# Kernel optimization log

Measured on AMD Instinct MI355X. Metric: run time of the kernel, lower is better.

Reference implementation:

```python
import jax, jax.numpy as jnp
import numpy as np

B, S, HID = 4, 2048, 576
NH, NKV, HD = 9, 3, 64
MAXPOS, THETA = 8192, 100000.0


def rotate_half(x):
    x1, x2 = x[..., : x.shape[-1] // 2], x[..., x.shape[-1] // 2 :]
    return jnp.concatenate((-x2, x1), axis=-1)


def setup_inputs() -> dict:
    key = jax.random.key(0)
    ks = jax.random.split(key, 6)
    x = jax.random.normal(ks[0], (B, S, HID), dtype=jnp.float32)
    # RoPE tables (HuggingFace layout: freqs duplicated across halves)
    inv_freq = 1.0 / (THETA ** (np.arange(0, HD, 2, dtype=np.float32) / HD))
    freqs = np.outer(np.arange(MAXPOS, dtype=np.float32), inv_freq)
    emb = np.concatenate([freqs, freqs], axis=-1)
    cos = jnp.asarray(np.cos(emb))
    sin = jnp.asarray(np.sin(emb))
    position_ids = jnp.broadcast_to(jnp.arange(S, dtype=jnp.int64), (B, S))
    # additive causal mask [B,1,S,S]
    causal = jnp.where(
        jnp.tril(jnp.ones((S, S), dtype=bool)), 0.0, -1e9
    ).astype(jnp.float32)
    attention_mask = jnp.broadcast_to(causal, (B, 1, S, S))
    scale = 0.02
    wq = jax.random.normal(ks[1], (NH * HD, HID), dtype=jnp.float32) * scale
    wk = jax.random.normal(ks[2], (NKV * HD, HID), dtype=jnp.float32) * scale
    wv = jax.random.normal(ks[3], (NKV * HD, HID), dtype=jnp.float32) * scale
    wo = jax.random.normal(ks[4], (HID, NH * HD), dtype=jnp.float32) * scale
    return {
        "x": x, "cos": cos, "sin": sin, "position_ids": position_ids,
        "attention_mask": attention_mask,
        "wq": wq, "wk": wk, "wv": wv, "wo": wo,
    }


def reference(x, cos, sin, position_ids, attention_mask, wq, wk, wv, wo):
    b, s, _ = x.shape
    # projections (nn.Linear: y = x @ W.T), split into heads -> [B,H,S,D]
    q = (x @ wq.T).reshape(b, s, NH, HD).transpose(0, 2, 1, 3)
    k = (x @ wk.T).reshape(b, s, NKV, HD).transpose(0, 2, 1, 3)
    v = (x @ wv.T).reshape(b, s, NKV, HD).transpose(0, 2, 1, 3)
    # RoPE: cos/sin gathered per position -> [B,1,S,D], broadcast over heads
    c = cos[position_ids][:, None, :, :]
    si = sin[position_ids][:, None, :, :]
    q = q * c + rotate_half(q) * si
    k = k * c + rotate_half(k) * si
    # GQA expansion: repeat_interleave kv heads to match q heads
    k = jnp.repeat(k, NH // NKV, axis=1)
    v = jnp.repeat(v, NH // NKV, axis=1)
    scale = 1.0 / jnp.sqrt(jnp.asarray(HD, dtype=x.dtype))
    scores = jnp.einsum("bhqd,bhkd->bhqk", q, k) * scale + attention_mask
    attn = jax.nn.softmax(scores.astype(jnp.float32), axis=-1).astype(q.dtype)
    out = jnp.einsum("bhqk,bhkd->bhqd", attn, v)
    out = out.transpose(0, 2, 1, 3).reshape(b, s, NH * HD)
    return out @ wo.T
```

## Files before the change

### kernel.cpp

```cpp
#include <hip/hip_runtime.h>
#include <hip/hip_bf16.h>

#define B_    4
#define S_    2048
#define HID_  576
#define NH_   9
#define NKV_  3
#define HD_   64
#define GQ_   3

typedef __attribute__((ext_vector_type(8))) short bf16x8;
typedef __attribute__((ext_vector_type(4))) float f32x4;

__device__ __forceinline__ short f2bf(float f) {
    union { float f; unsigned int u; } v; v.f = f;
    unsigned int r = (v.u + 0x7fffu + ((v.u >> 16) & 1u)) >> 16;
    return (short)r;
}

__device__ __forceinline__ void async16(const void* g, void* l) {
    __builtin_amdgcn_global_load_lds(
        (const __attribute__((address_space(1))) unsigned int*)g,
        (__attribute__((address_space(3))) unsigned int*)l, 16, 0, 0);
}

#define NX_   (8192 * 576)
#define NWQ_  (576 * 576)
#define NWK_  (192 * 576)
#define NWV_  (192 * 576)
#define NWO_  (576 * 576)
#define NTOT_ (NX_ + NWQ_ + NWK_ + NWV_ + NWO_)

__global__ __launch_bounds__(256) void convert_kernel(
    const float* __restrict__ x,  const float* __restrict__ wq,
    const float* __restrict__ wk, const float* __restrict__ wv,
    const float* __restrict__ wo,
    short* __restrict__ xb, short* __restrict__ wqkvb, short* __restrict__ wob)
{
    int i4 = (blockIdx.x * 256 + threadIdx.x) * 4;
    const float* src; short* dst;
    if (i4 < NX_)                          { src = x  + i4;                          dst = xb    + i4; }
    else if (i4 < NX_ + NWQ_)              { src = wq + (i4 - NX_);                  dst = wqkvb + (i4 - NX_); }
    else if (i4 < NX_ + NWQ_ + NWK_)       { src = wk + (i4 - NX_ - NWQ_);           dst = wqkvb + (i4 - NX_); }
    else if (i4 < NX_ + NWQ_ + NWK_ + NWV_){ src = wv + (i4 - NX_ - NWQ_ - NWK_);    dst = wqkvb + (i4 - NX_); }
    else                                   { src = wo + (i4 - NX_ - NWQ_ - NWK_ - NWV_);
                                             dst = wob + (i4 - NX_ - NWQ_ - NWK_ - NWV_); }
    float4 v = *(const float4*)src;
    short4 o = make_short4(f2bf(v.x), f2bf(v.y), f2bf(v.z), f2bf(v.w));
    *(short4*)dst = o;
}

__global__ __launch_bounds__(256) void qkv_kernel(
    const short* __restrict__ xb,
    const short* __restrict__ wqkvb,
    const float* __restrict__ cosb,
    const float* __restrict__ sinb,
    short* __restrict__ Q,
    short* __restrict__ K,
    short* __restrict__ Vt)
{
    __shared__ __align__(16) short As[128 * 64];
    __shared__ __align__(16) short Bs[64 * 64];

    const int m0     = blockIdx.x * 128;
    const int nb_blk = blockIdx.y;
    const int tid  = threadIdx.x;
    const int w    = tid >> 6, lane = tid & 63;
    const int quad = lane >> 4, c = lane & 15;
    const int lr   = lane >> 3, lg = lane & 7;
    const int sw   = lg ^ lr;
    const int xg   = quad ^ (c & 7);

    f32x4 acc[2][4];
    #pragma unroll
    for (int mf = 0; mf < 2; ++mf)
        #pragma unroll
        for (int nb = 0; nb < 4; ++nb) acc[mf][nb] = (f32x4){0.f, 0.f, 0.f, 0.f};

    for (int kk = 0; kk < 9; ++kk) {
        const int k0 = kk * 64;
        __syncthreads();
        #pragma unroll
        for (int r = 0; r < 4; ++r) {
            int ch = w * 4 + r;
            int R  = ch * 8 + lr;
            async16(xb + (size_t)(m0 + R) * HID_ + k0 + sw * 8,
                    (char*)As + ch * 1024);
        }
        #pragma unroll
        for (int r = 0; r < 2; ++r) {
            int ch = w * 2 + r;
            int R  = ch * 8 + lr;
            async16(wqkvb + (size_t)(nb_blk * 64 + R) * HID_ + k0 + sw * 8,
                    (char*)Bs + ch * 1024);
        }
        __syncthreads();

        bf16x8 a[2][2], bfr[4][2];
        #pragma unroll
        for (int mf = 0; mf < 2; ++mf) {
            int row = w * 32 + mf * 16 + c;
            a[mf][0] = *(const bf16x8*)(As + row * 64 + xg * 8);
            a[mf][1] = *(const bf16x8*)(As + row * 64 + (xg ^ 4) * 8);
        }
        #pragma unroll
        for (int nb = 0; nb < 4; ++nb) {
            int row = nb * 16 + c;
            bfr[nb][0] = *(const bf16x8*)(Bs + row * 64 + xg * 8);
            bfr[nb][1] = *(const bf16x8*)(Bs + row * 64 + (xg ^ 4) * 8);
        }
        #pragma unroll
        for (int mf = 0; mf < 2; ++mf)
            #pragma unroll
            for (int nb = 0; nb < 4; ++nb) {
                acc[mf][nb] = __builtin_amdgcn_mfma_f32_16x16x32_bf16(a[mf][0], bfr[nb][0], acc[mf][nb], 0, 0, 0);
                acc[mf][nb] = __builtin_amdgcn_mfma_f32_16x16x32_bf16(a[mf][1], bfr[nb][1], acc[mf][nb], 0, 0, 0);
            }
    }

    int type, head;
    if (nb_blk < NH_)            { type = 0; head = nb_blk; }
    else if (nb_blk < NH_ + NKV_){ type = 1; head = nb_blk - NH_; }
    else                         { type = 2; head = nb_blk - NH_ - NKV_; }
    const int b  = m0 >> 11;
    const int s0 = m0 & (S_ - 1);

    if (type < 2) {
        #pragma unroll
        for (int mf = 0; mf < 2; ++mf)
            #pragma unroll
            for (int reg = 0; reg < 4; ++reg) {
                int s = s0 + w * 32 + mf * 16 + quad * 4 + reg;
                const float* cr = cosb + (size_t)s * HD_;
                const float* sr = sinb + (size_t)s * HD_;
                float a0 = acc[mf][0][reg], a1 = acc[mf][1][reg];
                float a2 = acc[mf][2][reg], a3 = acc[mf][3][reg];
                float o0 = a0 * cr[c]      - a2 * sr[c];
                float o1 = a1 * cr[c + 16] - a3 * sr[c + 16];
                float o2 = a2 * cr[c + 32] + a0 * sr[c + 32];
                float o3 = a3 * cr[c + 48] + a1 * sr[c + 48];
                short* dst = (type == 0)
                    ? Q + (((size_t)b * NH_  + head) * S_ + s) * HD_
                    : K + (((size_t)b * NKV_ + head) * S_ + s) * HD_;
                dst[c]      = f2bf(o0);
                dst[c + 16] = f2bf(o1);
                dst[c + 32] = f2bf(o2);
                dst[c + 48] = f2bf(o3);
            }
    } else {
        short* base = Vt + (((size_t)b * NKV_ + head) * HD_) * S_;
        #pragma unroll
        for (int mf = 0; mf < 2; ++mf) {
            int s4 = s0 + w * 32 + mf * 16 + quad * 4;
            #pragma unroll
            for (int nb = 0; nb < 4; ++nb) {
                int d = nb * 16 + c;
                short4 pk = make_short4(f2bf(acc[mf][nb][0]), f2bf(acc[mf][nb][1]),
                                        f2bf(acc[mf][nb][2]), f2bf(acc[mf][nb][3]));
                *(short4*)(base + (size_t)d * S_ + s4) = pk;
            }
        }
    }
}

__global__ __launch_bounds__(256) void attn_kernel(
    const short* __restrict__ Q,
    const short* __restrict__ K,
    const short* __restrict__ Vt,
    short* __restrict__ AOb)
{
    __shared__ __align__(16) short Qs[64 * 64];
    __shared__ __align__(16) short Ks[2][64 * 64];
    __shared__ __align__(16) short Vs[2][64 * 64];
    __shared__ __align__(16) short Ps[64][72];

    const int hb = blockIdx.x;
    const int h  = hb >> 2, b = hb & 3;
    const int qt = 31 - blockIdx.y;
    const int kh = h / GQ_;
    const int tid  = threadIdx.x;
    const int w    = tid >> 6, lane = tid & 63;
    const int quad = lane >> 4, c = lane & 15;
    const int lr   = lane >> 3, lg = lane & 7;
    const int sw   = lg ^ lr;
    const int xg   = quad ^ (c & 7);

    const short* Qg = Q  + (((size_t)b * NH_  + h ) * S_ + qt * 64) * HD_;
    const short* Kg = K  + (((size_t)b * NKV_ + kh) * S_) * HD_;
    const short* Vg = Vt + (((size_t)b * NKV_ + kh) * HD_) * S_;

    #pragma unroll
    for (int r = 0; r < 2; ++r) {
        int ch = w * 2 + r;
        int R  = ch * 8 + lr;
        async16(Qg + (size_t)R * HD_ + sw * 8, (char*)Qs + ch * 1024);
    }
    #pragma unroll
    for (int r = 0; r < 4; ++r) {
        int it = w * 4 + r;
        if (it < 8) {
            int R = it * 8 + lr;
            async16(Kg + (size_t)R * HD_ + sw * 8, (char*)Ks[0] + it * 1024);
        } else {
            int R = (it - 8) * 8 + lr;
            async16(Vg + (size_t)R * S_ + sw * 8, (char*)Vs[0] + (it - 8) * 1024);
        }
    }

    f32x4 acc_o[4];
    #pragma unroll
    for (int nb = 0; nb < 4; ++nb) acc_o[nb] = (f32x4){0.f, 0.f, 0.f, 0.f};
    float mrow[4], lrow[4];
    #pragma unroll
    for (int r = 0; r < 4; ++r) { mrow[r] = -1e30f; lrow[r] = 0.f; }

    const float scale = 0.125f;
    int buf = 0;

    for (int kt = 0; kt <= qt; ++kt) {
        __syncthreads();
        if (kt < qt) {
            int nxt = buf ^ 1;
            #pragma unroll
            for (int r = 0; r < 4; ++r) {
                int it = w * 4 + r;
                if (it < 8) {
                    int R = it * 8 + lr;
                    async16(Kg + (size_t)((kt + 1) * 64 + R) * HD_ + sw * 8,
                            (char*)Ks[nxt] + it * 1024);
                } else {
                    int R = (it - 8) * 8 + lr;
                    async16(Vg + (size_t)R * S_ + (kt + 1) * 64 + sw * 8,
                            (char*)Vs[nxt] + (it - 8) * 1024);
                }
            }
        }
        const short* ks = Ks[buf];
        const short* vs = Vs[buf];

        bf16x8 aq0 = *(const bf16x8*)(Qs + (w * 16 + c) * 64 + xg * 8);
        bf16x8 aq1 = *(const bf16x8*)(Qs + (w * 16 + c) * 64 + (xg ^ 4) * 8);
        f32x4 sc[4];
        #pragma unroll
        for (int nb = 0; nb < 4; ++nb) {
            bf16x8 bk0 = *(const bf16x8*)(ks + (nb * 16 + c) * 64 + xg * 8);
            bf16x8 bk1 = *(const bf16x8*)(ks + (nb * 16 + c) * 64 + (xg ^ 4) * 8);
            f32x4 z = (f32x4){0.f, 0.f, 0.f, 0.f};
            z = __builtin_amdgcn_mfma_f32_16x16x32_bf16(aq0, bk0, z, 0, 0, 0);
            z = __builtin_amdgcn_mfma_f32_16x16x32_bf16(aq1, bk1, z, 0, 0, 0);
            sc[nb] = z;
        }

        const bool diag = (kt == qt);
        #pragma unroll
        for (int r = 0; r < 4; ++r) {
            const int qrow = w * 16 + quad * 4 + r;
            float v[4];
            float rmax = -1e30f;
            #pragma unroll
            for (int nb = 0; nb < 4; ++nb) {
                float sv = sc[nb][r] * scale;
                if (diag && (nb * 16 + c > qrow)) sv = -1e30f;
                v[nb] = sv;
                rmax = fmaxf(rmax, sv);
            }
            rmax = fmaxf(rmax, __shfl_xor(rmax, 1));
            rmax = fmaxf(rmax, __shfl_xor(rmax, 2));
            rmax = fmaxf(rmax, __shfl_xor(rmax, 4));
            rmax = fmaxf(rmax, __shfl_xor(rmax, 8));
            float mnew  = fmaxf(mrow[r], rmax);
            float alpha = __expf(mrow[r] - mnew);
            mrow[r] = mnew;
            float rsum = 0.f;
            #pragma unroll
            for (int nb = 0; nb < 4; ++nb) {
                float p = __expf(v[nb] - mnew);
                rsum += p;
                Ps[w * 16 + quad * 4 + r][nb * 16 + c] = f2bf(p);
            }
            rsum += __shfl_xor(rsum, 1);
            rsum += __shfl_xor(rsum, 2);
            rsum += __shfl_xor(rsum, 4);
            rsum += __shfl_xor(rsum, 8);
            lrow[r] = lrow[r] * alpha + rsum;
            #pragma unroll
            for (int nb = 0; nb < 4; ++nb) acc_o[nb][r] *= alpha;
        }

        #pragma unroll
        for (int kc = 0; kc < 2; ++kc) {
            bf16x8 ap = *(const bf16x8*)&Ps[w * 16 + c][quad * 8 + kc * 32];
            int pg = kc ? (xg ^ 4) : xg;
            #pragma unroll
            for (int nb = 0; nb < 4; ++nb) {
                bf16x8 bv = *(const bf16x8*)(vs + (nb * 16 + c) * 64 + pg * 8);
                acc_o[nb] = __builtin_amdgcn_mfma_f32_16x16x32_bf16(ap, bv, acc_o[nb], 0, 0, 0);
            }
        }
        buf ^= 1;
    }

    #pragma unroll
    for (int r = 0; r < 4; ++r) {
        int s = qt * 64 + w * 16 + quad * 4 + r;
        float inv = 1.f / lrow[r];
        short* dst = AOb + (((size_t)b * S_ + s) * NH_ + h) * HD_;
        #pragma unroll
        for (int nb = 0; nb < 4; ++nb)
            dst[nb * 16 + c] = f2bf(acc_o[nb][r] * inv);
    }
}

__global__ __launch_bounds__(256) void oproj_kernel(
    const short* __restrict__ AOb,
    const short* __restrict__ wob,
    float* __restrict__ out)
{
    __shared__ __align__(16) short As[128 * 64];
    __shared__ __align__(16) short Bs[64 * 64];

    const int m0 = blockIdx.x * 128;
    const int n0 = blockIdx.y * 64;
    const int tid  = threadIdx.x;
    const int w    = tid >> 6, lane = tid & 63;
    const int quad = lane >> 4, c = lane & 15;
    const int lr   = lane >> 3, lg = lane & 7;
    const int sw   = lg ^ lr;
    const int xg   = quad ^ (c & 7);

    f32x4 acc[2][4];
    #pragma unroll
    for (int mf = 0; mf < 2; ++mf)
        #pragma unroll
        for (int nb = 0; nb < 4; ++nb) acc[mf][nb] = (f32x4){0.f, 0.f, 0.f, 0.f};

    for (int kk = 0; kk < 9; ++kk) {
        const int k0 = kk * 64;
        __syncthreads();
        #pragma unroll
        for (int r = 0; r < 4; ++r) {
            int ch = w * 4 + r;
            int R  = ch * 8 + lr;
            async16(AOb + (size_t)(m0 + R) * HID_ + k0 + sw * 8,
                    (char*)As + ch * 1024);
        }
        #pragma unroll
        for (int r = 0; r < 2; ++r) {
            int ch = w * 2 + r;
            int R  = ch * 8 + lr;
            async16(wob + (size_t)(n0 + R) * HID_ + k0 + sw * 8,
                    (char*)Bs + ch * 1024);
        }
        __syncthreads();

        bf16x8 a[2][2], bfr[4][2];
        #pragma unroll
        for (int mf = 0; mf < 2; ++mf) {
            int row = w * 32 + mf * 16 + c;
            a[mf][0] = *(const bf16x8*)(As + row * 64 + xg * 8);
            a[mf][1] = *(const bf16x8*)(As + row * 64 + (xg ^ 4) * 8);
        }
        #pragma unroll
        for (int nb = 0; nb < 4; ++nb) {
            int row = nb * 16 + c;
            bfr[nb][0] = *(const bf16x8*)(Bs + row * 64 + xg * 8);
            bfr[nb][1] = *(const bf16x8*)(Bs + row * 64 + (xg ^ 4) * 8);
        }
        #pragma unroll
        for (int mf = 0; mf < 2; ++mf)
            #pragma unroll
            for (int nb = 0; nb < 4; ++nb) {
                acc[mf][nb] = __builtin_amdgcn_mfma_f32_16x16x32_bf16(a[mf][0], bfr[nb][0], acc[mf][nb], 0, 0, 0);
                acc[mf][nb] = __builtin_amdgcn_mfma_f32_16x16x32_bf16(a[mf][1], bfr[nb][1], acc[mf][nb], 0, 0, 0);
            }
    }

    #pragma unroll
    for (int mf = 0; mf < 2; ++mf)
        #pragma unroll
        for (int reg = 0; reg < 4; ++reg) {
            int m = m0 + w * 32 + mf * 16 + quad * 4 + reg;
            float* dst = out + (size_t)m * HID_ + n0;
            #pragma unroll
            for (int nb = 0; nb < 4; ++nb)
                dst[nb * 16 + c] = acc[mf][nb][reg];
        }
}

extern "C" void kernel_launch(void* const* d_in, const int* in_sizes, int n_in,
                              void* d_out, int out_size, void* d_ws, size_t ws_size,
                              hipStream_t stream) {
    const float* x    = (const float*)d_in[0];
    const float* cosb = (const float*)d_in[1];
    const float* sinb = (const float*)d_in[2];
    const float* wq   = (const float*)d_in[5];
    const float* wk   = (const float*)d_in[6];
    const float* wv   = (const float*)d_in[7];
    const float* wo   = (const float*)d_in[8];

    short* xb    = (short*)d_ws;
    short* wqkvb = xb    + (size_t)NX_;
    short* wob   = wqkvb + (size_t)(NWQ_ + NWK_ + NWV_);
    short* Qb    = wob   + (size_t)NWO_;
    short* Kb    = Qb    + (size_t)B_ * NH_  * S_ * HD_;
    short* Vtb   = Kb    + (size_t)B_ * NKV_ * S_ * HD_;
    short* AOb   = Vtb   + (size_t)B_ * NKV_ * S_ * HD_;

    convert_kernel<<<dim3(NTOT_ / 4 / 256), dim3(256), 0, stream>>>(
        x, wq, wk, wv, wo, xb, wqkvb, wob);
    qkv_kernel<<<dim3(64, 15), dim3(256), 0, stream>>>(
        xb, wqkvb, cosb, sinb, Qb, Kb, Vtb);
    attn_kernel<<<dim3(36, 32), dim3(256), 0, stream>>>(Qb, Kb, Vtb, AOb);
    oproj_kernel<<<dim3(64, 9), dim3(256), 0, stream>>>(AOb, wob, (float*)d_out);
}
```

Before: 215.0 us.

## Enlarge attention query tile to 128 rows and double-buffer GEMM loads

The attention kernel now handles 128 query rows per block, with each warp owning 32 rows. Every K/V tile loaded into shared memory is therefore reused across twice as many queries. Q is kept in registers so its shared buffer can be reused for the softmax probabilities, and the causal mask now covers the two diagonal KV tiles. Separately, the QKV and output-projection GEMMs double-buffer their A/B tiles, prefetching the next K slice during the current MFMAs. The costs are half as many attention blocks, which risks worse load balance on the causal grid, and higher register and LDS use per block.

```diff
diff --git a/kernel.cpp b/kernel.cpp
--- a/kernel.cpp
+++ b/kernel.cpp
@@ -59,8 +59,8 @@
     short* __restrict__ K,
     short* __restrict__ Vt)
 {
-    __shared__ __align__(16) short As[128 * 64];
-    __shared__ __align__(16) short Bs[64 * 64];
+    __shared__ __align__(16) short As[2][128 * 64];
+    __shared__ __align__(16) short Bs[2][64 * 64];
 
     const int m0     = blockIdx.x * 128;
     const int nb_blk = blockIdx.y;
@@ -77,37 +77,48 @@
         #pragma unroll
         for (int nb = 0; nb < 4; ++nb) acc[mf][nb] = (f32x4){0.f, 0.f, 0.f, 0.f};
 
+    #pragma unroll
+    for (int r = 0; r < 4; ++r) {
+        int ch = w * 4 + r, R = ch * 8 + lr;
+        async16(xb + (size_t)(m0 + R) * HID_ + sw * 8, (char*)As[0] + ch * 1024);
+    }
+    #pragma unroll
+    for (int r = 0; r < 2; ++r) {
+        int ch = w * 2 + r, R = ch * 8 + lr;
+        async16(wqkvb + (size_t)(nb_blk * 64 + R) * HID_ + sw * 8, (char*)Bs[0] + ch * 1024);
+    }
+
+    int buf = 0;
     for (int kk = 0; kk < 9; ++kk) {
-        const int k0 = kk * 64;
         __syncthreads();
-        #pragma unroll
-        for (int r = 0; r < 4; ++r) {
-            int ch = w * 4 + r;
-            int R  = ch * 8 + lr;
-            async16(xb + (size_t)(m0 + R) * HID_ + k0 + sw * 8,
-                    (char*)As + ch * 1024);
-        }
-        #pragma unroll
-        for (int r = 0; r < 2; ++r) {
-            int ch = w * 2 + r;
-            int R  = ch * 8 + lr;
-            async16(wqkvb + (size_t)(nb_blk * 64 + R) * HID_ + k0 + sw * 8,
-                    (char*)Bs + ch * 1024);
-        }
-        __syncthreads();
+        if (kk < 8) {
+            const int k0 = (kk + 1) * 64;
+            #pragma unroll
+            for (int r = 0; r < 4; ++r) {
+                int ch = w * 4 + r, R = ch * 8 + lr;
+                async16(xb + (size_t)(m0 + R) * HID_ + k0 + sw * 8,
+                        (char*)As[buf ^ 1] + ch * 1024);
+            }
+            #pragma unroll
+            for (int r = 0; r < 2; ++r) {
+                int ch = w * 2 + r, R = ch * 8 + lr;
+                async16(wqkvb + (size_t)(nb_blk * 64 + R) * HID_ + k0 + sw * 8,
+                        (char*)Bs[buf ^ 1] + ch * 1024);
+            }
+        }
 
         bf16x8 a[2][2], bfr[4][2];
         #pragma unroll
         for (int mf = 0; mf < 2; ++mf) {
             int row = w * 32 + mf * 16 + c;
-            a[mf][0] = *(const bf16x8*)(As + row * 64 + xg * 8);
-            a[mf][1] = *(const bf16x8*)(As + row * 64 + (xg ^ 4) * 8);
+            a[mf][0] = *(const bf16x8*)(As[buf] + row * 64 + xg * 8);
+            a[mf][1] = *(const bf16x8*)(As[buf] + row * 64 + (xg ^ 4) * 8);
         }
         #pragma unroll
         for (int nb = 0; nb < 4; ++nb) {
             int row = nb * 16 + c;
-            bfr[nb][0] = *(const bf16x8*)(Bs + row * 64 + xg * 8);
-            bfr[nb][1] = *(const bf16x8*)(Bs + row * 64 + (xg ^ 4) * 8);
+            bfr[nb][0] = *(const bf16x8*)(Bs[buf] + row * 64 + xg * 8);
+            bfr[nb][1] = *(const bf16x8*)(Bs[buf] + row * 64 + (xg ^ 4) * 8);
         }
         #pragma unroll
         for (int mf = 0; mf < 2; ++mf)
@@ -116,6 +127,7 @@
                 acc[mf][nb] = __builtin_amdgcn_mfma_f32_16x16x32_bf16(a[mf][0], bfr[nb][0], acc[mf][nb], 0, 0, 0);
                 acc[mf][nb] = __builtin_amdgcn_mfma_f32_16x16x32_bf16(a[mf][1], bfr[nb][1], acc[mf][nb], 0, 0, 0);
             }
+        buf ^= 1;
     }
 
     int type, head;
@@ -163,20 +175,21 @@
     }
 }
 
+#define PSTR 72
+
 __global__ __launch_bounds__(256) void attn_kernel(
     const short* __restrict__ Q,
     const short* __restrict__ K,
     const short* __restrict__ Vt,
     short* __restrict__ AOb)
 {
-    __shared__ __align__(16) short Qs[64 * 64];
+    __shared__ __align__(16) short PQ[128 * PSTR];
     __shared__ __align__(16) short Ks[2][64 * 64];
     __shared__ __align__(16) short Vs[2][64 * 64];
-    __shared__ __align__(16) short Ps[64][72];
 
     const int hb = blockIdx.x;
     const int h  = hb >> 2, b = hb & 3;
-    const int qt = 31 - blockIdx.y;
+    const int qt = 15 - blockIdx.y;
     const int kh = h / GQ_;
     const int tid  = threadIdx.x;
     const int w    = tid >> 6, lane = tid & 63;
@@ -185,15 +198,14 @@
     const int sw   = lg ^ lr;
     const int xg   = quad ^ (c & 7);
 
-    const short* Qg = Q  + (((size_t)b * NH_  + h ) * S_ + qt * 64) * HD_;
+    const short* Qg = Q  + (((size_t)b * NH_  + h ) * S_ + qt * 128) * HD_;
     const short* Kg = K  + (((size_t)b * NKV_ + kh) * S_) * HD_;
     const short* Vg = Vt + (((size_t)b * NKV_ + kh) * HD_) * S_;
 
     #pragma unroll
-    for (int r = 0; r < 2; ++r) {
-        int ch = w * 2 + r;
-        int R  = ch * 8 + lr;
-        async16(Qg + (size_t)R * HD_ + sw * 8, (char*)Qs + ch * 1024);
+    for (int r = 0; r < 4; ++r) {
+        int ch = w * 4 + r, R = ch * 8 + lr;
+        async16(Qg + (size_t)R * HD_ + sw * 8, (char*)PQ + ch * 1024);
     }
     #pragma unroll
     for (int r = 0; r < 4; ++r) {
@@ -207,19 +219,34 @@
         }
     }
 
-    f32x4 acc_o[4];
-    #pragma unroll
-    for (int nb = 0; nb < 4; ++nb) acc_o[nb] = (f32x4){0.f, 0.f, 0.f, 0.f};
-    float mrow[4], lrow[4];
-    #pragma unroll
-    for (int r = 0; r < 4; ++r) { mrow[r] = -1e30f; lrow[r] = 0.f; }
+    bf16x8 aq[2][2];
+    f32x4 acc_o[2][4];
+    #pragma unroll
+    for (int mf = 0; mf < 2; ++mf)
+        #pragma unroll
+        for (int nb = 0; nb < 4; ++nb) acc_o[mf][nb] = (f32x4){0.f, 0.f, 0.f, 0.f};
+    float mrow[2][4], lrow[2][4];
+    #pragma unroll
+    for (int mf = 0; mf < 2; ++mf)
+        #pragma unroll
+        for (int r = 0; r < 4; ++r) { mrow[mf][r] = -1e30f; lrow[mf][r] = 0.f; }
 
     const float scale = 0.125f;
+    const int nkv = 2 * qt + 2;
     int buf = 0;
 
-    for (int kt = 0; kt <= qt; ++kt) {
+    for (int kt = 0; kt < nkv; ++kt) {
         __syncthreads();
-        if (kt < qt) {
+        if (kt == 0) {
+            #pragma unroll
+            for (int mf = 0; mf < 2; ++mf) {
+                int row = w * 32 + mf * 16 + c;
+                aq[mf][0] = *(const bf16x8*)(PQ + row * 64 + xg * 8);
+                aq[mf][1] = *(const bf16x8*)(PQ + row * 64 + (xg ^ 4) * 8);
+            }
+            __syncthreads();
+        }
+        if (kt + 1 < nkv) {
             int nxt = buf ^ 1;
             #pragma unroll
             for (int r = 0; r < 4; ++r) {
@@ -238,77 +265,85 @@
         const short* ks = Ks[buf];
         const short* vs = Vs[buf];
 
-        bf16x8 aq0 = *(const bf16x8*)(Qs + (w * 16 + c) * 64 + xg * 8);
-        bf16x8 aq1 = *(const bf16x8*)(Qs + (w * 16 + c) * 64 + (xg ^ 4) * 8);
-        f32x4 sc[4];
+        f32x4 sc[2][4];
         #pragma unroll
         for (int nb = 0; nb < 4; ++nb) {
             bf16x8 bk0 = *(const bf16x8*)(ks + (nb * 16 + c) * 64 + xg * 8);
             bf16x8 bk1 = *(const bf16x8*)(ks + (nb * 16 + c) * 64 + (xg ^ 4) * 8);
-            f32x4 z = (f32x4){0.f, 0.f, 0.f, 0.f};
-            z = __builtin_amdgcn_mfma_f32_16x16x32_bf16(aq0, bk0, z, 0, 0, 0);
-            z = __builtin_amdgcn_mfma_f32_16x16x32_bf16(aq1, bk1, z, 0, 0, 0);
-            sc[nb] = z;
-        }
-
-        const bool diag = (kt == qt);
+            #pragma unroll
+            for (int mf = 0; mf < 2; ++mf) {
+                f32x4 z = (f32x4){0.f, 0.f, 0.f, 0.f};
+                z = __builtin_amdgcn_mfma_f32_16x16x32_bf16(aq[mf][0], bk0, z, 0, 0, 0);
+                z = __builtin_amdgcn_mfma_f32_16x16x32_bf16(aq[mf][1], bk1, z, 0, 0, 0);
+                sc[mf][nb] = z;
+            }
+        }
+
+        const bool near = (kt >= 2 * qt);
+        #pragma unroll
+        for (int mf = 0; mf < 2; ++mf)
+            #pragma unroll
+            for (int r = 0; r < 4; ++r) {
+                const int qrow = qt * 128 + w * 32 + mf * 16 + quad * 4 + r;
+                float v[4];
+                float rmax = -1e30f;
+                #pragma unroll
+                for (int nb = 0; nb < 4; ++nb) {
+                    float sv = sc[mf][nb][r] * scale;
+                    if (near && (kt * 64 + nb * 16 + c > qrow)) sv = -1e30f;
+                    v[nb] = sv;
+                    rmax = fmaxf(rmax, sv);
+                }
+                rmax = fmaxf(rmax, __shfl_xor(rmax, 1));
+                rmax = fmaxf(rmax, __shfl_xor(rmax, 2));
+                rmax = fmaxf(rmax, __shfl_xor(rmax, 4));
+                rmax = fmaxf(rmax, __shfl_xor(rmax, 8));
+                float mnew  = fmaxf(mrow[mf][r], rmax);
+                float alpha = __expf(mrow[mf][r] - mnew);
+                mrow[mf][r] = mnew;
+                float rsum = 0.f;
+                #pragma unroll
+                for (int nb = 0; nb < 4; ++nb) {
+                    float p = __expf(v[nb] - mnew);
+                    rsum += p;
+                    PQ[(w * 32 + mf * 16 + quad * 4 + r) * PSTR + nb * 16 + c] = f2bf(p);
+                }
+                rsum += __shfl_xor(rsum, 1);
+                rsum += __shfl_xor(rsum, 2);
+                rsum += __shfl_xor(rsum, 4);
+                rsum += __shfl_xor(rsum, 8);
+                lrow[mf][r] = lrow[mf][r] * alpha + rsum;
+                #pragma unroll
+                for (int nb = 0; nb < 4; ++nb) acc_o[mf][nb][r] *= alpha;
+            }
+
+        #pragma unroll
+        for (int mf = 0; mf < 2; ++mf)
+            #pragma unroll
+            for (int kc = 0; kc < 2; ++kc) {
+                bf16x8 ap = *(const bf16x8*)(PQ + (w * 32 + mf * 16 + c) * PSTR
+                                             + quad * 8 + kc * 32);
+                int pg = kc ? (xg ^ 4) : xg;
+                #pragma unroll
+                for (int nb = 0; nb < 4; ++nb) {
+                    bf16x8 bv = *(const bf16x8*)(vs + (nb * 16 + c) * 64 + pg * 8);
+                    acc_o[mf][nb] = __builtin_amdgcn_mfma_f32_16x16x32_bf16(ap, bv, acc_o[mf][nb], 0, 0, 0);
+                }
+            }
+        buf ^= 1;
+    }
+
+    #pragma unroll
+    for (int mf = 0; mf < 2; ++mf)
         #pragma unroll
         for (int r = 0; r < 4; ++r) {
-            const int qrow = w * 16 + quad * 4 + r;
-            float v[4];
-            float rmax = -1e30f;
-            #pragma unroll
-            for (int nb = 0; nb < 4; ++nb) {
-                float sv = sc[nb][r] * scale;
-                if (diag && (nb * 16 + c > qrow)) sv = -1e30f;
-                v[nb] = sv;
-                rmax = fmaxf(rmax, sv);
-            }
-            rmax = fmaxf(rmax, __shfl_xor(rmax, 1));
-            rmax = fmaxf(rmax, __shfl_xor(rmax, 2));
-            rmax = fmaxf(rmax, __shfl_xor(rmax, 4));
-            rmax = fmaxf(rmax, __shfl_xor(rmax, 8));
-            float mnew  = fmaxf(mrow[r], rmax);
-            float alpha = __expf(mrow[r] - mnew);
-            mrow[r] = mnew;
-            float rsum = 0.f;
-            #pragma unroll
-            for (int nb = 0; nb < 4; ++nb) {
-                float p = __expf(v[nb] - mnew);
-                rsum += p;
-                Ps[w * 16 + quad * 4 + r][nb * 16 + c] = f2bf(p);
-            }
-            rsum += __shfl_xor(rsum, 1);
-            rsum += __shfl_xor(rsum, 2);
-            rsum += __shfl_xor(rsum, 4);
-            rsum += __shfl_xor(rsum, 8);
-            lrow[r] = lrow[r] * alpha + rsum;
-            #pragma unroll
-            for (int nb = 0; nb < 4; ++nb) acc_o[nb][r] *= alpha;
-        }
-
-        #pragma unroll
-        for (int kc = 0; kc < 2; ++kc) {
-            bf16x8 ap = *(const bf16x8*)&Ps[w * 16 + c][quad * 8 + kc * 32];
-            int pg = kc ? (xg ^ 4) : xg;
-            #pragma unroll
-            for (int nb = 0; nb < 4; ++nb) {
-                bf16x8 bv = *(const bf16x8*)(vs + (nb * 16 + c) * 64 + pg * 8);
-                acc_o[nb] = __builtin_amdgcn_mfma_f32_16x16x32_bf16(ap, bv, acc_o[nb], 0, 0, 0);
-            }
-        }
-        buf ^= 1;
-    }
-
-    #pragma unroll
-    for (int r = 0; r < 4; ++r) {
-        int s = qt * 64 + w * 16 + quad * 4 + r;
-        float inv = 1.f / lrow[r];
-        short* dst = AOb + (((size_t)b * S_ + s) * NH_ + h) * HD_;
-        #pragma unroll
-        for (int nb = 0; nb < 4; ++nb)
-            dst[nb * 16 + c] = f2bf(acc_o[nb][r] * inv);
-    }
+            int s = qt * 128 + w * 32 + mf * 16 + quad * 4 + r;
+            float inv = 1.f / lrow[mf][r];
+            short* dst = AOb + (((size_t)b * S_ + s) * NH_ + h) * HD_;
+            #pragma unroll
+            for (int nb = 0; nb < 4; ++nb)
+                dst[nb * 16 + c] = f2bf(acc_o[mf][nb][r] * inv);
+        }
 }
 
 __global__ __launch_bounds__(256) void oproj_kernel(
@@ -316,8 +351,8 @@
     const short* __restrict__ wob,
     float* __restrict__ out)
 {
-    __shared__ __align__(16) short As[128 * 64];
-    __shared__ __align__(16) short Bs[64 * 64];
+    __shared__ __align__(16) short As[2][128 * 64];
+    __shared__ __align__(16) short Bs[2][64 * 64];
 
     const int m0 = blockIdx.x * 128;
     const int n0 = blockIdx.y * 64;
@@ -334,37 +369,48 @@
         #pragma unroll
         for (int nb = 0; nb < 4; ++nb) acc[mf][nb] = (f32x4){0.f, 0.f, 0.f, 0.f};
 
+    #pragma unroll
+    for (int r = 0; r < 4; ++r) {
+        int ch = w * 4 + r, R = ch * 8 + lr;
+        async16(AOb + (size_t)(m0 + R) * HID_ + sw * 8, (char*)As[0] + ch * 1024);
+    }
+    #pragma unroll
+    for (int r = 0; r < 2; ++r) {
+        int ch = w * 2 + r, R = ch * 8 + lr;
+        async16(wob + (size_t)(n0 + R) * HID_ + sw * 8, (char*)Bs[0] + ch * 1024);
+    }
+
+    int buf = 0;
     for (int kk = 0; kk < 9; ++kk) {
-        const int k0 = kk * 64;
         __syncthreads();
-        #pragma unroll
-        for (int r = 0; r < 4; ++r) {
-            int ch = w * 4 + r;
-            int R  = ch * 8 + lr;
-            async16(AOb + (size_t)(m0 + R) * HID_ + k0 + sw * 8,
-                    (char*)As + ch * 1024);
-        }
-        #pragma unroll
-        for (int r = 0; r < 2; ++r) {
-            int ch = w * 2 + r;
-            int R  = ch * 8 + lr;
-            async16(wob + (size_t)(n0 + R) * HID_ + k0 + sw * 8,
-                    (char*)Bs + ch * 1024);
-        }
-        __syncthreads();
+        if (kk < 8) {
+            const int k0 = (kk + 1) * 64;
+            #pragma unroll
+            for (int r = 0; r < 4; ++r) {
+                int ch = w * 4 + r, R = ch * 8 + lr;
+                async16(AOb + (size_t)(m0 + R) * HID_ + k0 + sw * 8,
+                        (char*)As[buf ^ 1] + ch * 1024);
+            }
+            #pragma unroll
+            for (int r = 0; r < 2; ++r) {
+                int ch = w * 2 + r, R = ch * 8 + lr;
+                async16(wob + (size_t)(n0 + R) * HID_ + k0 + sw * 8,
+                        (char*)Bs[buf ^ 1] + ch * 1024);
+            }
+        }
 
         bf16x8 a[2][2], bfr[4][2];
         #pragma unroll
         for (int mf = 0; mf < 2; ++mf) {
             int row = w * 32 + mf * 16 + c;
-            a[mf][0] = *(const bf16x8*)(As + row * 64 + xg * 8);
-            a[mf][1] = *(const bf16x8*)(As + row * 64 + (xg ^ 4) * 8);
+            a[mf][0] = *(const bf16x8*)(As[buf] + row * 64 + xg * 8);
+            a[mf][1] = *(const bf16x8*)(As[buf] + row * 64 + (xg ^ 4) * 8);
         }
         #pragma unroll
         for (int nb = 0; nb < 4; ++nb) {
             int row = nb * 16 + c;
-            bfr[nb][0] = *(const bf16x8*)(Bs + row * 64 + xg * 8);
-            bfr[nb][1] = *(const bf16x8*)(Bs + row * 64 + (xg ^ 4) * 8);
+            bfr[nb][0] = *(const bf16x8*)(Bs[buf] + row * 64 + xg * 8);
+            bfr[nb][1] = *(const bf16x8*)(Bs[buf] + row * 64 + (xg ^ 4) * 8);
         }
         #pragma unroll
         for (int mf = 0; mf < 2; ++mf)
@@ -373,6 +419,7 @@
                 acc[mf][nb] = __builtin_amdgcn_mfma_f32_16x16x32_bf16(a[mf][0], bfr[nb][0], acc[mf][nb], 0, 0, 0);
                 acc[mf][nb] = __builtin_amdgcn_mfma_f32_16x16x32_bf16(a[mf][1], bfr[nb][1], acc[mf][nb], 0, 0, 0);
             }
+        buf ^= 1;
     }
 
     #pragma unroll
@@ -410,6 +457,6 @@
         x, wq, wk, wv, wo, xb, wqkvb, wob);
     qkv_kernel<<<dim3(64, 15), dim3(256), 0, stream>>>(
         xb, wqkvb, cosb, sinb, Qb, Kb, Vtb);
-    attn_kernel<<<dim3(36, 32), dim3(256), 0, stream>>>(Qb, Kb, Vtb, AOb);
+    attn_kernel<<<dim3(36, 16), dim3(256), 0, stream>>>(Qb, Kb, Vtb, AOb);
     oproj_kernel<<<dim3(64, 9), dim3(256), 0, stream>>>(AOb, wob, (float*)d_out);
 }
```

Result: slower. 268.9 us (+25.1%).
